# Performance work log

Measured on AMD Instinct MI355X. Metric: run time of the kernel, lower is better.

The kernel has to match this reference:

```python
import jax, jax.numpy as jnp
import numpy as np

B, C_IN, C_MID, C_OUT, H, W = 16, 128, 128, 128, 128, 128
DN = ('NCHW', 'OIHW', 'NCHW')


def conv1x1(x, w, b):
    y = jax.lax.conv_general_dilated(x, w, (1, 1), 'VALID', dimension_numbers=DN)
    return y + b[None, :, None, None]


def dwconv3(x, w, b):
    # depthwise 3x3, padding=1, groups = channels
    y = jax.lax.conv_general_dilated(x, w, (1, 1), ((1, 1), (1, 1)),
                                     feature_group_count=x.shape[1],
                                     dimension_numbers=DN)
    return y + b[None, :, None, None]


def setup_inputs() -> dict:
    key = jax.random.key(0)
    ks = jax.random.split(key, 15)
    s = 0.05
    return {
        'x':   jax.random.normal(ks[0], (B, C_IN, H, W), jnp.float32),
        'qw':  jax.random.normal(ks[1], (C_MID, C_IN, 1, 1), jnp.float32) * s,
        'qb':  jax.random.normal(ks[2], (C_MID,), jnp.float32) * s,
        'qdw': jax.random.normal(ks[3], (C_MID, 1, 3, 3), jnp.float32) * s,
        'qdb': jax.random.normal(ks[4], (C_MID,), jnp.float32) * s,
        'kw':  jax.random.normal(ks[5], (C_MID, C_IN, 1, 1), jnp.float32) * s,
        'kb':  jax.random.normal(ks[6], (C_MID,), jnp.float32) * s,
        'kdw': jax.random.normal(ks[7], (C_MID, 1, 3, 3), jnp.float32) * s,
        'kdb': jax.random.normal(ks[8], (C_MID,), jnp.float32) * s,
        'vw':  jax.random.normal(ks[9], (C_MID, C_IN, 1, 1), jnp.float32) * s,
        'vb':  jax.random.normal(ks[10], (C_MID,), jnp.float32) * s,
        'vdw': jax.random.normal(ks[11], (C_MID, 1, 3, 3), jnp.float32) * s,
        'vdb': jax.random.normal(ks[12], (C_MID,), jnp.float32) * s,
        'aw':  jax.random.normal(ks[13], (C_OUT, C_MID, 1, 1), jnp.float32) * s,
        'ab':  jax.random.normal(ks[14], (C_OUT,), jnp.float32) * s,
    }


def reference(x, qw, qb, qdw, qdb, kw, kb, kdw, kdb, vw, vb, vdw, vdb, aw, ab):
    b, c, h, w = x.shape
    q = dwconv3(conv1x1(x, qw, qb), qdw, qdb)
    k = dwconv3(conv1x1(x, kw, kb), kdw, kdb)
    v = dwconv3(conv1x1(x, vw, vb), vdw, vdb)
    # b c h w -> b c (h w)
    q = q.reshape(b, -1, h * w)
    k = k.reshape(b, -1, h * w)
    v = v.reshape(b, -1, h * w)
    # L2-normalize over spatial dim (torch F.normalize: x / max(||x||, eps))
    eps = 1e-12
    q = q / jnp.maximum(jnp.linalg.norm(q, axis=-1, keepdims=True), eps)
    k = k / jnp.maximum(jnp.linalg.norm(k, axis=-1, keepdims=True), eps)
    # channel-wise attention: [b, c, c]
    a = jax.nn.softmax(jnp.einsum('bcn,bdn->bcd', q, k), axis=-1)
    out = jnp.einsum('bcd,bdn->bcn', a, v).reshape(b, -1, h, w)
    return conv1x1(out, aw, ab)
```

## Files before the change

### kernel.cpp

```cpp
#include <hip/hip_runtime.h>

typedef unsigned short u16;
typedef unsigned int u32;
typedef __attribute__((ext_vector_type(8))) __bf16 bf16x8;
typedef __attribute__((ext_vector_type(4))) float f32x4;
typedef __attribute__((ext_vector_type(4))) u32 u32x4;
typedef __attribute__((ext_vector_type(2))) u32 u32x2;

#define HW 16384
#define C 128
#define NB 16
#define LSTR 136

__device__ __forceinline__ u16 f2bf(float f) {
    __bf16 h = (__bf16)f;
    union { __bf16 h; u16 u; } c; c.h = h; return c.u;
}
__device__ __forceinline__ float bf2f(u16 u) {
    union { u32 i; float f; } c; c.i = ((u32)u) << 16; return c.f;
}

__device__ __forceinline__ bf16x8 load_wrow(const float* p) {
    f32x4 a = *(const f32x4*)p, b = *(const f32x4*)(p + 4);
    bf16x8 r;
    #pragma unroll
    for (int i = 0; i < 4; ++i) { r[i] = (__bf16)a[i]; r[i + 4] = (__bf16)b[i]; }
    return r;
}
__device__ __forceinline__ bf16x8 load_wrow(const u16* p) {
    return *(const bf16x8*)p;
}

template <typename WT>
__device__ __forceinline__ void mfma_tile(
    const WT* __restrict__ W, const u16* lds,
    f32x4 (&acc)[2][8], int wave, int m_lo, int quad)
{
    #pragma unroll
    for (int mt = 0; mt < 2; ++mt)
        #pragma unroll
        for (int nt = 0; nt < 8; ++nt) {
            f32x4 z = {0.f, 0.f, 0.f, 0.f};
            acc[mt][nt] = z;
        }
    #pragma unroll
    for (int ks = 0; ks < 4; ++ks) {
        const int k0 = ks * 32 + quad * 8;
        bf16x8 af[2];
        #pragma unroll
        for (int mt = 0; mt < 2; ++mt) {
            int m = wave * 32 + mt * 16 + m_lo;
            af[mt] = load_wrow(W + (size_t)m * 128 + k0);
        }
        #pragma unroll
        for (int nt = 0; nt < 8; ++nt) {
            int n  = nt * 16 + m_lo;
            int cs = (ks * 4 + quad) ^ ((n >> 2) & 7);
            bf16x8 bfrag = *(const bf16x8*)(lds + n * LSTR + cs * 8);
            #pragma unroll
            for (int mt = 0; mt < 2; ++mt)
                acc[mt][nt] = __builtin_amdgcn_mfma_f32_16x16x32_bf16(
                    bfrag, af[mt], acc[mt][nt], 0, 0, 0);
        }
    }
}

__global__ __launch_bounds__(256) void k_conv_qkv(
    float* __restrict__ x,
    const float* __restrict__ qw, const float* __restrict__ qbi,
    const float* __restrict__ kw, const float* __restrict__ kbi,
    const float* __restrict__ vw, const float* __restrict__ vbi,
    u16* __restrict__ qpl, u16* __restrict__ kpl)
{
    __shared__ __align__(16) u16 lds[128 * LSTR];
    const int tid  = threadIdx.x;
    const int lane = tid & 63;
    const int wave = tid >> 6;
    const int m_lo = lane & 15;
    const int quad = lane >> 4;
    const int b  = blockIdx.z;
    const int n0 = blockIdx.x * 128;
    float* Xb = x + (size_t)b * C * HW;

    #pragma unroll
    for (int r = 0; r < 2; ++r) {
        int idx = tid + 256 * r;
        int n4  = idx & 31;
        int kc  = idx >> 5;
        const float* src = Xb + (size_t)(kc * 8) * HW + n0 + n4 * 4;
        f32x4 v[8];
        #pragma unroll
        for (int j = 0; j < 8; ++j) v[j] = *(const f32x4*)(src + (size_t)j * HW);
        #pragma unroll
        for (int t = 0; t < 4; ++t) {
            union { u16 u[8]; u32x4 q; } e;
            #pragma unroll
            for (int j = 0; j < 8; ++j) e.u[j] = f2bf(v[j][t]);
            int row = n4 * 4 + t;
            int cs  = kc ^ (n4 & 7);
            *(u32x4*)(lds + row * LSTR + cs * 8) = e.q;
        }
    }
    __syncthreads();

    f32x4 acc[2][8];

    #pragma unroll 1
    for (int s = 0; s < 2; ++s) {
        const float* W    = s ? kw : qw;
        const float* bias = s ? kbi : qbi;
        u16* Y = (s ? kpl : qpl) + (size_t)b * C * HW;
        mfma_tile(W, lds, acc, wave, m_lo, quad);
        #pragma unroll
        for (int mt = 0; mt < 2; ++mt) {
            int m = wave * 32 + mt * 16 + m_lo;
            float bm = bias[m];
            u16* rowp = Y + (size_t)m * HW + n0 + quad * 4;
            #pragma unroll
            for (int nt = 0; nt < 8; ++nt) {
                u32x2 pr;
                pr.x = (u32)f2bf(acc[mt][nt][0] + bm) | ((u32)f2bf(acc[mt][nt][1] + bm) << 16);
                pr.y = (u32)f2bf(acc[mt][nt][2] + bm) | ((u32)f2bf(acc[mt][nt][3] + bm) << 16);
                *(u32x2*)(rowp + nt * 16) = pr;
            }
        }
    }

    mfma_tile(vw, lds, acc, wave, m_lo, quad);
    #pragma unroll
    for (int mt = 0; mt < 2; ++mt) {
        int m = wave * 32 + mt * 16 + m_lo;
        float bm = vbi[m];
        float* rowp = Xb + (size_t)m * HW + n0 + quad * 4;
        #pragma unroll
        for (int nt = 0; nt < 8; ++nt) {
            f32x4 o = acc[mt][nt];
            o[0] += bm; o[1] += bm; o[2] += bm; o[3] += bm;
            *(f32x4*)(rowp + nt * 16) = o;
        }
    }
}

__global__ __launch_bounds__(256) void k_dw_qk(
    u16* __restrict__ qpl, u16* __restrict__ kpl,
    const float* __restrict__ qdw, const float* __restrict__ qdb,
    const float* __restrict__ kdw, const float* __restrict__ kdb,
    float* __restrict__ norm2)
{
    __shared__ __align__(16) u16 pl[HW];
    __shared__ float red[256];
    int pid = blockIdx.x;
    int s = pid >> 11, bc = pid & 2047, c = bc & 127;
    u16* plane = (s ? kpl : qpl) + (size_t)bc * HW;
    const float* dw = (s ? kdw : qdw) + c * 9;
    float bias = (s ? kdb : qdb)[c];
    int tid = threadIdx.x;

    #pragma unroll
    for (int i = 0; i < 8; ++i) {
        int idx = tid + 256 * i;
        *(u32x4*)(pl + idx * 8) = *(const u32x4*)(plane + idx * 8);
    }
    float w[9];
    #pragma unroll
    for (int j = 0; j < 9; ++j) w[j] = dw[j];
    __syncthreads();

    float ssq = 0.f;
    for (int i = 0; i < 16; ++i) {
        int p0 = (tid + 256 * i) * 4;
        int py = p0 >> 7, px0 = p0 & 127;
        float nb[3][6];
        #pragma unroll
        for (int dy = 0; dy < 3; ++dy) {
            int yy = py + dy - 1;
            bool yok = (yy >= 0) && (yy < 128);
            int ya = yok ? yy : 0;
            #pragma unroll
            for (int j = 0; j < 6; ++j) {
                int xx = px0 + j - 1;
                bool ok = yok && (xx >= 0) && (xx < 128);
                int xa = (xx >= 0 && xx < 128) ? xx : 0;
                float vv = bf2f(pl[ya * 128 + xa]);
                nb[dy][j] = ok ? vv : 0.f;
            }
        }
        u16 o[4];
        #pragma unroll
        for (int t = 0; t < 4; ++t) {
            float acc = bias;
            #pragma unroll
            for (int dy = 0; dy < 3; ++dy)
                #pragma unroll
                for (int dx = 0; dx < 3; ++dx)
                    acc += w[dy * 3 + dx] * nb[dy][t + dx];
            ssq += acc * acc;
            o[t] = f2bf(acc);
        }
        u32x2 pr;
        pr.x = (u32)o[0] | ((u32)o[1] << 16);
        pr.y = (u32)o[2] | ((u32)o[3] << 16);
        *(u32x2*)(plane + p0) = pr;
    }
    red[tid] = ssq;
    __syncthreads();
    for (int off = 128; off > 0; off >>= 1) {
        if (tid < off) red[tid] += red[tid + off];
        __syncthreads();
    }
    if (tid == 0) norm2[s * (NB * C) + bc] = red[0];
}

__global__ __launch_bounds__(256) void k_gram(
    const u16* __restrict__ q, const u16* __restrict__ k, float* __restrict__ G)
{
    int kz = blockIdx.x, nz = blockIdx.y, b = blockIdx.z;
    const u16* qb = q + (size_t)b * C * HW;
    const u16* kb = k + (size_t)b * C * HW;
    int lane = threadIdx.x & 63, wave = threadIdx.x >> 6;
    int m_lo = lane & 15, quad = lane >> 4;
    f32x4 acc[2][4];
    #pragma unroll
    for (int mt = 0; mt < 2; ++mt)
        #pragma unroll
        for (int nt = 0; nt < 4; ++nt) {
            f32x4 z = {0.f, 0.f, 0.f, 0.f};
            acc[mt][nt] = z;
        }
    for (int step = 0; step < 32; ++step) {
        int kk = kz * 1024 + step * 32 + quad * 8;
        bf16x8 a0 = *(const bf16x8*)(qb + (size_t)(wave * 32 + m_lo) * HW + kk);
        bf16x8 a1 = *(const bf16x8*)(qb + (size_t)(wave * 32 + 16 + m_lo) * HW + kk);
        #pragma unroll
        for (int nt = 0; nt < 4; ++nt) {
            bf16x8 bf = *(const bf16x8*)(kb + (size_t)(nz * 64 + nt * 16 + m_lo) * HW + kk);
            acc[0][nt] = __builtin_amdgcn_mfma_f32_16x16x32_bf16(a0, bf, acc[0][nt], 0, 0, 0);
            acc[1][nt] = __builtin_amdgcn_mfma_f32_16x16x32_bf16(a1, bf, acc[1][nt], 0, 0, 0);
        }
    }
    float* Gb = G + (size_t)b * C * C;
    #pragma unroll
    for (int mt = 0; mt < 2; ++mt)
        #pragma unroll
        for (int nt = 0; nt < 4; ++nt)
            #pragma unroll
            for (int r = 0; r < 4; ++r) {
                int m = wave * 32 + mt * 16 + quad * 4 + r;
                int n = nz * 64 + nt * 16 + m_lo;
                atomicAdd(&Gb[m * C + n], acc[mt][nt][r]);
            }
}

__global__ __launch_bounds__(128) void k_softmax(float* __restrict__ G, const float* __restrict__ norm2)
{
    __shared__ float red[128];
    int c = blockIdx.x, b = blockIdx.y, d = threadIdx.x;
    float* row = G + ((size_t)b * C + c) * C;
    float nq = fmaxf(sqrtf(norm2[b * C + c]), 1e-12f);
    float nk = fmaxf(sqrtf(norm2[NB * C + b * C + d]), 1e-12f);
    float sv = row[d] / (nq * nk);
    red[d] = sv; __syncthreads();
    for (int off = 64; off > 0; off >>= 1) {
        if (d < off) red[d] = fmaxf(red[d], red[d + off]);
        __syncthreads();
    }
    float mx = red[0]; __syncthreads();
    float e = __expf(sv - mx);
    red[d] = e; __syncthreads();
    for (int off = 64; off > 0; off >>= 1) {
        if (d < off) red[d] += red[d + off];
        __syncthreads();
    }
    row[d] = e / red[0];
}

__global__ __launch_bounds__(256) void k_mproj(
    const float* __restrict__ G, const float* __restrict__ aw, u16* __restrict__ M)
{
    __shared__ float As[128 * 16];
    int b = blockIdx.y, d0 = blockIdx.x * 16, tid = threadIdx.x;
    const float* A = G + (size_t)b * C * C;
    #pragma unroll
    for (int i = 0; i < 8; ++i) {
        int idx = tid + 256 * i;
        int cc = idx >> 4, dd = idx & 15;
        As[idx] = A[cc * C + d0 + dd];
    }
    __syncthreads();
    #pragma unroll
    for (int i = 0; i < 8; ++i) {
        int idx = tid + 256 * i;
        int oo = idx >> 4, dd = idx & 15;
        float s = 0.f;
        for (int cc = 0; cc < 128; ++cc)
            s += aw[oo * C + cc] * As[cc * 16 + dd];
        M[((size_t)b * C + oo) * C + d0 + dd] = f2bf(s);
    }
}

__global__ __launch_bounds__(256) void k_out(
    const u16* __restrict__ M, const float* __restrict__ v,
    const float* __restrict__ vdw, const float* __restrict__ vdb,
    const float* __restrict__ ab, float* __restrict__ out)
{
    __shared__ __align__(16) u16 lds[128 * LSTR];
    const int tid  = threadIdx.x;
    const int lane = tid & 63;
    const int wave = tid >> 6;
    const int m_lo = lane & 15;
    const int quad = lane >> 4;
    const int b   = blockIdx.z;
    const int row = blockIdx.x;
    const int n0  = row * 128;
    const float* Vb = v + (size_t)b * C * HW;

    int rs[3] = { row > 0 ? row - 1 : 0, row, row < 127 ? row + 1 : 127 };
    float rmask[3] = { row > 0 ? 1.f : 0.f, 1.f, row < 127 ? 1.f : 0.f };

    #pragma unroll
    for (int it = 0; it < 2; ++it) {
        int idx = tid + 256 * it;
        int n8 = idx & 15;
        int kq = idx >> 4;
        int p0 = n8 * 8;
        float lm  = (n8 > 0)  ? 1.f : 0.f;
        float rmx = (n8 < 15) ? 1.f : 0.f;
        int pL = (n8 > 0)  ? p0 - 1 : 0;
        int pR = (n8 < 15) ? p0 + 8 : 127;
        float o[4][8];
        #pragma unroll
        for (int j = 0; j < 4; ++j) {
            int ch = kq * 4 + j;
            const float* pw = vdw + ch * 9;
            float bias = vdb[ch];
            #pragma unroll
            for (int t = 0; t < 8; ++t) o[j][t] = bias;
            const float* plane = Vb + (size_t)ch * HW;
            #pragma unroll
            for (int dy = 0; dy < 3; ++dy) {
                const float* rp = plane + rs[dy] * 128;
                float rm = rmask[dy];
                float win[10];
                f32x4 m0 = *(const f32x4*)(rp + p0);
                f32x4 m1 = *(const f32x4*)(rp + p0 + 4);
                win[0] = rp[pL] * lm * rm;
                win[9] = rp[pR] * rmx * rm;
                #pragma unroll
                for (int q2 = 0; q2 < 4; ++q2) { win[1 + q2] = m0[q2] * rm; win[5 + q2] = m1[q2] * rm; }
                float w0 = pw[dy * 3 + 0], w1 = pw[dy * 3 + 1], w2 = pw[dy * 3 + 2];
                #pragma unroll
                for (int t = 0; t < 8; ++t)
                    o[j][t] += w0 * win[t] + w1 * win[t + 1] + w2 * win[t + 2];
            }
        }
        #pragma unroll
        for (int t = 0; t < 8; ++t) {
            int rw  = p0 + t;
            int n4t = (rw >> 2) & 31;
            int cs  = (kq >> 1) ^ (n4t & 7);
            u32x2 e;
            e.x = (u32)f2bf(o[0][t]) | ((u32)f2bf(o[1][t]) << 16);
            e.y = (u32)f2bf(o[2][t]) | ((u32)f2bf(o[3][t]) << 16);
            *(u32x2*)(lds + rw * LSTR + cs * 8 + (kq & 1) * 4) = e;
        }
    }
    __syncthreads();

    f32x4 acc[2][8];
    mfma_tile(M + (size_t)b * C * C, lds, acc, wave, m_lo, quad);

    float* Ob = out + (size_t)b * C * HW;
    #pragma unroll
    for (int mt = 0; mt < 2; ++mt) {
        int m = wave * 32 + mt * 16 + m_lo;
        float bm = ab[m];
        float* rowp = Ob + (size_t)m * HW + n0 + quad * 4;
        #pragma unroll
        for (int nt = 0; nt < 8; ++nt) {
            f32x4 o = acc[mt][nt];
            o[0] += bm; o[1] += bm; o[2] += bm; o[3] += bm;
            *(f32x4*)(rowp + nt * 16) = o;
        }
    }
}

extern "C" void kernel_launch(void* const* d_in, const int* in_sizes, int n_in,
                              void* d_out, int out_size, void* d_ws, size_t ws_size,
                              hipStream_t stream)
{
    float* x         = (float*)d_in[0];
    const float* qw  = (const float*)d_in[1];
    const float* qbi = (const float*)d_in[2];
    const float* qdw = (const float*)d_in[3];
    const float* qdb = (const float*)d_in[4];
    const float* kw  = (const float*)d_in[5];
    const float* kbi = (const float*)d_in[6];
    const float* kdw = (const float*)d_in[7];
    const float* kdb = (const float*)d_in[8];
    const float* vw  = (const float*)d_in[9];
    const float* vbi = (const float*)d_in[10];
    const float* vdw = (const float*)d_in[11];
    const float* vdb = (const float*)d_in[12];
    const float* aw  = (const float*)d_in[13];
    const float* ab  = (const float*)d_in[14];

    u16* qpl = (u16*)d_out;
    u16* kpl = qpl + (size_t)NB * C * HW;

    float* G     = (float*)d_ws;
    float* norm2 = G + (size_t)NB * C * C;
    u16*   M     = (u16*)(norm2 + 2 * NB * C);

    hipMemsetAsync(G, 0, (size_t)NB * C * C * sizeof(float), stream);

    k_conv_qkv<<<dim3(HW / 128, 1, NB), 256, 0, stream>>>(x, qw, qbi, kw, kbi, vw, vbi, qpl, kpl);
    k_dw_qk<<<dim3(2 * NB * C), 256, 0, stream>>>(qpl, kpl, qdw, qdb, kdw, kdb, norm2);
    k_gram<<<dim3(16, 2, NB), 256, 0, stream>>>(qpl, kpl, G);
    k_softmax<<<dim3(C, NB), 128, 0, stream>>>(G, norm2);
    k_mproj<<<dim3(8, NB), 256, 0, stream>>>(G, aw, M);
    k_out<<<dim3(HW / 128, 1, NB), 256, 0, stream>>>(M, x, vdw, vdb, ab, (float*)d_out);
}
```

Baseline: 554.7 us.

## Pre-convert conv weights to bf16, preload A fragments, widen dwconv, split gram further

```diff
diff --git a/kernel.cpp b/kernel.cpp
--- a/kernel.cpp
+++ b/kernel.cpp
@@ -10,7 +10,7 @@
 #define HW 16384
 #define C 128
 #define NB 16
-#define LSTR 136
+#define LSTR 128
 
 __device__ __forceinline__ u16 f2bf(float f) {
     __bf16 h = (__bf16)f;
@@ -19,22 +19,24 @@
 __device__ __forceinline__ float bf2f(u16 u) {
     union { u32 i; float f; } c; c.i = ((u32)u) << 16; return c.f;
 }
-
-__device__ __forceinline__ bf16x8 load_wrow(const float* p) {
-    f32x4 a = *(const f32x4*)p, b = *(const f32x4*)(p + 4);
-    bf16x8 r;
-    #pragma unroll
-    for (int i = 0; i < 4; ++i) { r[i] = (__bf16)a[i]; r[i + 4] = (__bf16)b[i]; }
-    return r;
-}
-__device__ __forceinline__ bf16x8 load_wrow(const u16* p) {
-    return *(const bf16x8*)p;
-}
-
-template <typename WT>
-__device__ __forceinline__ void mfma_tile(
-    const WT* __restrict__ W, const u16* lds,
-    f32x4 (&acc)[2][8], int wave, int m_lo, int quad)
+__device__ __forceinline__ float bflo(u32 w) { return bf2f((u16)(w & 0xffffu)); }
+__device__ __forceinline__ float bfhi(u32 w) { return bf2f((u16)(w >> 16)); }
+
+__device__ __forceinline__ void load_af(
+    const u16* __restrict__ W, bf16x8 (&af)[2][4], int wave, int m_lo, int quad)
+{
+    #pragma unroll
+    for (int mt = 0; mt < 2; ++mt)
+        #pragma unroll
+        for (int ks = 0; ks < 4; ++ks) {
+            int m = wave * 32 + mt * 16 + m_lo;
+            af[mt][ks] = *(const bf16x8*)(W + (size_t)m * 128 + ks * 32 + quad * 8);
+        }
+}
+
+__device__ __forceinline__ void mfma_tile2(
+    const bf16x8 (&af)[2][4], const u16* lds,
+    f32x4 (&acc)[2][8], int m_lo, int quad)
 {
     #pragma unroll
     for (int mt = 0; mt < 2; ++mt)
@@ -45,31 +47,39 @@
         }
     #pragma unroll
     for (int ks = 0; ks < 4; ++ks) {
-        const int k0 = ks * 32 + quad * 8;
-        bf16x8 af[2];
-        #pragma unroll
-        for (int mt = 0; mt < 2; ++mt) {
-            int m = wave * 32 + mt * 16 + m_lo;
-            af[mt] = load_wrow(W + (size_t)m * 128 + k0);
-        }
         #pragma unroll
         for (int nt = 0; nt < 8; ++nt) {
             int n  = nt * 16 + m_lo;
             int cs = (ks * 4 + quad) ^ ((n >> 2) & 7);
             bf16x8 bfrag = *(const bf16x8*)(lds + n * LSTR + cs * 8);
-            #pragma unroll
-            for (int mt = 0; mt < 2; ++mt)
-                acc[mt][nt] = __builtin_amdgcn_mfma_f32_16x16x32_bf16(
-                    bfrag, af[mt], acc[mt][nt], 0, 0, 0);
-        }
-    }
-}
-
-__global__ __launch_bounds__(256) void k_conv_qkv(
-    float* __restrict__ x,
-    const float* __restrict__ qw, const float* __restrict__ qbi,
-    const float* __restrict__ kw, const float* __restrict__ kbi,
-    const float* __restrict__ vw, const float* __restrict__ vbi,
+            acc[0][nt] = __builtin_amdgcn_mfma_f32_16x16x32_bf16(bfrag, af[0][ks], acc[0][nt], 0, 0, 0);
+            acc[1][nt] = __builtin_amdgcn_mfma_f32_16x16x32_bf16(bfrag, af[1][ks], acc[1][nt], 0, 0, 0);
+        }
+    }
+}
+
+__global__ __launch_bounds__(256) void k_wcvt(
+    const float* __restrict__ qw, const float* __restrict__ kw,
+    const float* __restrict__ vw, u16* __restrict__ wbf)
+{
+    int m = blockIdx.x;
+    const float* src = m == 0 ? qw : (m == 1 ? kw : vw);
+    u16* dst = wbf + (size_t)m * 16384;
+    #pragma unroll
+    for (int i = 0; i < 16; ++i) {
+        int idx = threadIdx.x + 256 * i;
+        f32x4 v = *(const f32x4*)(src + idx * 4);
+        u32x2 p;
+        p.x = (u32)f2bf(v[0]) | ((u32)f2bf(v[1]) << 16);
+        p.y = (u32)f2bf(v[2]) | ((u32)f2bf(v[3]) << 16);
+        *(u32x2*)(dst + idx * 4) = p;
+    }
+}
+
+__global__ __launch_bounds__(256, 4) void k_conv_qkv(
+    float* __restrict__ x, const u16* __restrict__ wbf,
+    const float* __restrict__ qbi, const float* __restrict__ kbi,
+    const float* __restrict__ vbi,
     u16* __restrict__ qpl, u16* __restrict__ kpl)
 {
     __shared__ __align__(16) u16 lds[128 * LSTR];
@@ -103,30 +113,49 @@
     }
     __syncthreads();
 
+    const u16* wq = wbf;
+    const u16* wk = wbf + 16384;
+    const u16* wv = wbf + 32768;
+    u16* Yq = qpl + (size_t)b * C * HW;
+    u16* Yk = kpl + (size_t)b * C * HW;
+
+    bf16x8 af[2][4];
     f32x4 acc[2][8];
 
-    #pragma unroll 1
-    for (int s = 0; s < 2; ++s) {
-        const float* W    = s ? kw : qw;
-        const float* bias = s ? kbi : qbi;
-        u16* Y = (s ? kpl : qpl) + (size_t)b * C * HW;
-        mfma_tile(W, lds, acc, wave, m_lo, quad);
-        #pragma unroll
-        for (int mt = 0; mt < 2; ++mt) {
-            int m = wave * 32 + mt * 16 + m_lo;
-            float bm = bias[m];
-            u16* rowp = Y + (size_t)m * HW + n0 + quad * 4;
-            #pragma unroll
-            for (int nt = 0; nt < 8; ++nt) {
-                u32x2 pr;
-                pr.x = (u32)f2bf(acc[mt][nt][0] + bm) | ((u32)f2bf(acc[mt][nt][1] + bm) << 16);
-                pr.y = (u32)f2bf(acc[mt][nt][2] + bm) | ((u32)f2bf(acc[mt][nt][3] + bm) << 16);
-                *(u32x2*)(rowp + nt * 16) = pr;
-            }
-        }
-    }
-
-    mfma_tile(vw, lds, acc, wave, m_lo, quad);
+    load_af(wq, af, wave, m_lo, quad);
+    mfma_tile2(af, lds, acc, m_lo, quad);
+    load_af(wk, af, wave, m_lo, quad);
+    #pragma unroll
+    for (int mt = 0; mt < 2; ++mt) {
+        int m = wave * 32 + mt * 16 + m_lo;
+        float bm = qbi[m];
+        u16* rowp = Yq + (size_t)m * HW + n0 + quad * 4;
+        #pragma unroll
+        for (int nt = 0; nt < 8; ++nt) {
+            u32x2 pr;
+            pr.x = (u32)f2bf(acc[mt][nt][0] + bm) | ((u32)f2bf(acc[mt][nt][1] + bm) << 16);
+            pr.y = (u32)f2bf(acc[mt][nt][2] + bm) | ((u32)f2bf(acc[mt][nt][3] + bm) << 16);
+            *(u32x2*)(rowp + nt * 16) = pr;
+        }
+    }
+
+    mfma_tile2(af, lds, acc, m_lo, quad);
+    load_af(wv, af, wave, m_lo, quad);
+    #pragma unroll
+    for (int mt = 0; mt < 2; ++mt) {
+        int m = wave * 32 + mt * 16 + m_lo;
+        float bm = kbi[m];
+        u16* rowp = Yk + (size_t)m * HW + n0 + quad * 4;
+        #pragma unroll
+        for (int nt = 0; nt < 8; ++nt) {
+            u32x2 pr;
+            pr.x = (u32)f2bf(acc[mt][nt][0] + bm) | ((u32)f2bf(acc[mt][nt][1] + bm) << 16);
+            pr.y = (u32)f2bf(acc[mt][nt][2] + bm) | ((u32)f2bf(acc[mt][nt][3] + bm) << 16);
+            *(u32x2*)(rowp + nt * 16) = pr;
+        }
+    }
+
+    mfma_tile2(af, lds, acc, m_lo, quad);
     #pragma unroll
     for (int mt = 0; mt < 2; ++mt) {
         int m = wave * 32 + mt * 16 + m_lo;
@@ -147,7 +176,7 @@
     const float* __restrict__ kdw, const float* __restrict__ kdb,
     float* __restrict__ norm2)
 {
-    __shared__ __align__(16) u16 pl[HW];
+    __shared__ __align__(16) u16 pl[HW + 8];
     __shared__ float red[256];
     int pid = blockIdx.x;
     int s = pid >> 11, bc = pid & 2047, c = bc & 127;
@@ -161,33 +190,44 @@
         int idx = tid + 256 * i;
         *(u32x4*)(pl + idx * 8) = *(const u32x4*)(plane + idx * 8);
     }
+    if (tid < 4) *(u32*)(pl + HW + tid * 2) = 0u;
     float w[9];
     #pragma unroll
     for (int j = 0; j < 9; ++j) w[j] = dw[j];
     __syncthreads();
 
     float ssq = 0.f;
-    for (int i = 0; i < 16; ++i) {
-        int p0 = (tid + 256 * i) * 4;
+    #pragma unroll 1
+    for (int i = 0; i < 8; ++i) {
+        int p0 = (tid + 256 * i) * 8;
         int py = p0 >> 7, px0 = p0 & 127;
-        float nb[3][6];
+        bool lok = px0 > 0, rok = px0 < 120;
+        float nb[3][10];
         #pragma unroll
         for (int dy = 0; dy < 3; ++dy) {
             int yy = py + dy - 1;
             bool yok = (yy >= 0) && (yy < 128);
             int ya = yok ? yy : 0;
-            #pragma unroll
-            for (int j = 0; j < 6; ++j) {
-                int xx = px0 + j - 1;
-                bool ok = yok && (xx >= 0) && (xx < 128);
-                int xa = (xx >= 0 && xx < 128) ? xx : 0;
-                float vv = bf2f(pl[ya * 128 + xa]);
-                nb[dy][j] = ok ? vv : 0.f;
-            }
-        }
-        u16 o[4];
-        #pragma unroll
-        for (int t = 0; t < 4; ++t) {
+            const u16* rp = pl + ya * 128;
+            u32x2 L  = *(const u32x2*)(rp + (lok ? px0 - 4 : 0));
+            u32x2 M0 = *(const u32x2*)(rp + px0);
+            u32x2 M1 = *(const u32x2*)(rp + px0 + 4);
+            u32x2 R  = *(const u32x2*)(rp + px0 + 8);
+            float rm = yok ? 1.f : 0.f;
+            nb[dy][0] = (lok && yok) ? bfhi(L.y) : 0.f;
+            nb[dy][1] = bflo(M0.x) * rm;
+            nb[dy][2] = bfhi(M0.x) * rm;
+            nb[dy][3] = bflo(M0.y) * rm;
+            nb[dy][4] = bfhi(M0.y) * rm;
+            nb[dy][5] = bflo(M1.x) * rm;
+            nb[dy][6] = bfhi(M1.x) * rm;
+            nb[dy][7] = bflo(M1.y) * rm;
+            nb[dy][8] = bfhi(M1.y) * rm;
+            nb[dy][9] = (rok && yok) ? bflo(R.x) : 0.f;
+        }
+        u16 o[8];
+        #pragma unroll
+        for (int t = 0; t < 8; ++t) {
             float acc = bias;
             #pragma unroll
             for (int dy = 0; dy < 3; ++dy)
@@ -197,10 +237,12 @@
             ssq += acc * acc;
             o[t] = f2bf(acc);
         }
-        u32x2 pr;
+        u32x4 pr;
         pr.x = (u32)o[0] | ((u32)o[1] << 16);
         pr.y = (u32)o[2] | ((u32)o[3] << 16);
-        *(u32x2*)(plane + p0) = pr;
+        pr.z = (u32)o[4] | ((u32)o[5] << 16);
+        pr.w = (u32)o[6] | ((u32)o[7] << 16);
+        *(u32x4*)(plane + p0) = pr;
     }
     red[tid] = ssq;
     __syncthreads();
@@ -227,8 +269,9 @@
             f32x4 z = {0.f, 0.f, 0.f, 0.f};
             acc[mt][nt] = z;
         }
-    for (int step = 0; step < 32; ++step) {
-        int kk = kz * 1024 + step * 32 + quad * 8;
+    #pragma unroll 2
+    for (int step = 0; step < 16; ++step) {
+        int kk = kz * 512 + step * 32 + quad * 8;
         bf16x8 a0 = *(const bf16x8*)(qb + (size_t)(wave * 32 + m_lo) * HW + kk);
         bf16x8 a1 = *(const bf16x8*)(qb + (size_t)(wave * 32 + 16 + m_lo) * HW + kk);
         #pragma unroll
@@ -298,7 +341,7 @@
     }
 }
 
-__global__ __launch_bounds__(256) void k_out(
+__global__ __launch_bounds__(256, 4) void k_out(
     const u16* __restrict__ M, const float* __restrict__ v,
     const float* __restrict__ vdw, const float* __restrict__ vdb,
     const float* __restrict__ ab, float* __restrict__ out)
@@ -366,8 +409,10 @@
     }
     __syncthreads();
 
+    bf16x8 af[2][4];
     f32x4 acc[2][8];
-    mfma_tile(M + (size_t)b * C * C, lds, acc, wave, m_lo, quad);
+    load_af(M + (size_t)b * C * C, af, wave, m_lo, quad);
+    mfma_tile2(af, lds, acc, m_lo, quad);
 
     float* Ob = out + (size_t)b * C * HW;
     #pragma unroll
@@ -410,12 +455,14 @@
     float* G     = (float*)d_ws;
     float* norm2 = G + (size_t)NB * C * C;
     u16*   M     = (u16*)(norm2 + 2 * NB * C);
+    u16*   wbf   = M + (size_t)NB * C * C;
 
     hipMemsetAsync(G, 0, (size_t)NB * C * C * sizeof(float), stream);
 
-    k_conv_qkv<<<dim3(HW / 128, 1, NB), 256, 0, stream>>>(x, qw, qbi, kw, kbi, vw, vbi, qpl, kpl);
+    k_wcvt<<<dim3(3), 256, 0, stream>>>(qw, kw, vw, wbf);
+    k_conv_qkv<<<dim3(HW / 128, 1, NB), 256, 0, stream>>>(x, wbf, qbi, kbi, vbi, qpl, kpl);
     k_dw_qk<<<dim3(2 * NB * C), 256, 0, stream>>>(qpl, kpl, qdw, qdb, kdw, kdb, norm2);
-    k_gram<<<dim3(16, 2, NB), 256, 0, stream>>>(qpl, kpl, G);
+    k_gram<<<dim3(32, 2, NB), 256, 0, stream>>>(qpl, kpl, G);
     k_softmax<<<dim3(C, NB), 128, 0, stream>>>(G, norm2);
     k_mproj<<<dim3(8, NB), 256, 0, stream>>>(G, aw, M);
     k_out<<<dim3(HW / 128, 1, NB), 256, 0, stream>>>(M, x, vdw, vdb, ab, (float*)d_out);
```

After: 926.1 us. 67.0% more time.
